# Kernel tuning notes

Measured on AMD Instinct MI355X. Metric: run time of the kernel, lower is better.

## Reference

```python
import jax, jax.numpy as jnp
import numpy as np

B, H, FEAT = 16384, 256, 256
GX, GY, SW = 70, 70, 2


def setup_inputs() -> dict:
    key = jax.random.key(0)
    ks = jax.random.split(key, 10)
    stdv = 1.0 / np.sqrt(H)
    feats = jax.random.normal(ks[0], (B, FEAT), dtype=jnp.float32)
    coords = jax.random.randint(ks[1], (B, 2), 0, 64).astype(jnp.float32)
    input_tensor = jnp.concatenate([feats, coords], axis=1)  # [B, FEAT+2]
    hidden = jax.random.normal(ks[2], (B, H), dtype=jnp.float32)
    u = lambda k, shp: jax.random.uniform(k, shp, jnp.float32, -stdv, stdv)
    return {
        "input_tensor": input_tensor,
        "hidden": hidden,
        "w_ih": u(ks[3], (4 * H, FEAT)),
        "b_ih": u(ks[4], (4 * H,)),
        "w_hh": u(ks[5], (4 * H, H)),
        "b_hh": u(ks[6], (4 * H,)),
        "w_out": u(ks[7], (H, 2 * H)),
        "b_out": u(ks[8], (H,)),
        "memory": jax.random.normal(ks[9], (GX, GY, H), dtype=jnp.float32) * 0.1,
    }


def reference(input_tensor, hidden, w_ih, b_ih, w_hh, b_hh, w_out, b_out, memory):
    feature = input_tensor[:, :-2]
    grid = input_tensor[:, -2:].astype(jnp.int32) + SW  # [B,2]

    gi = feature @ w_ih.T + b_ih  # [B,4H]
    gh = hidden @ w_hh.T + b_hh   # [B,4H]
    i_r, i_i, i_n, i_s = jnp.split(gi, 4, axis=1)
    h_r, h_i, h_n, h_s = jnp.split(gh, 4, axis=1)

    resetgate = jax.nn.sigmoid(i_r + h_r)
    updategate = jax.nn.sigmoid(i_i + h_i)
    spatialgate = jax.nn.sigmoid(i_s + h_s)
    newgate = jnp.tanh(i_n + resetgate * h_n)

    # gather (2*SW+1)^2 neighborhood per sample from spatial memory
    gx = jnp.clip(grid[:, 0], 0, GX - 1)
    gy = jnp.clip(grid[:, 1], 0, GY - 1)
    off = jnp.arange(-SW, SW + 1)  # [K]
    xi = jnp.clip(gx[:, None] + off[None, :], 0, GX - 1)  # [B,K]
    yi = jnp.clip(gy[:, None] + off[None, :], 0, GY - 1)  # [B,K]
    K = 2 * SW + 1
    x_flat = jnp.broadcast_to(xi[:, :, None], (xi.shape[0], K, K)).reshape(xi.shape[0], -1)
    y_flat = jnp.broadcast_to(yi[:, None, :], (yi.shape[0], K, K)).reshape(yi.shape[0], -1)
    context = memory[x_flat, y_flat]  # [B, K*K, H]

    # attention (query is detached in original)
    q = jax.lax.stop_gradient(newgate)  # [B,H]
    attn = jnp.einsum('bh,bkh->bk', q, context)  # [B, K*K]
    attn = jnp.where(attn == 0, -jnp.inf, attn)
    w = jax.nn.softmax(attn, axis=1)
    w = jnp.where(jnp.isnan(w), 0.0, w)
    mix = jnp.einsum('bk,bkh->bh', w, context)  # [B,H]
    combined = jnp.concatenate([mix, q], axis=1)  # [B,2H]
    atten_cs = jnp.tanh(combined @ w_out.T + b_out)  # [B,H]

    curr_state = newgate + spatialgate * atten_cs
    output = curr_state + updategate * (hidden - curr_state)
    return output
```

## Files before the change

kernel.cpp:

```cpp
#include <hip/hip_runtime.h>
#include <stdint.h>

#define B_N 16384
#define H_N 256
#define IN_W 258
#define GX_N 70
#define GY_N 70
#define SW_N 2
#define KK_N 25

typedef __bf16 bf16x8 __attribute__((ext_vector_type(8)));
typedef __bf16 bf16x4 __attribute__((ext_vector_type(4)));
typedef __bf16 bf16x2 __attribute__((ext_vector_type(2)));
typedef float f32x4 __attribute__((ext_vector_type(4)));

#define AS1 __attribute__((address_space(1)))
#define AS3 __attribute__((address_space(3)))

static __device__ __forceinline__ void gload16(const void* g, void* l) {
    __builtin_amdgcn_global_load_lds((const AS1 uint32_t*)g, (AS3 uint32_t*)l, 16, 0, 0);
}

#define E_AB   8388608ULL
#define E_WIH  8650752ULL
#define E_WHH  8912896ULL
#define E_WOUT 9043968ULL
#define E_COMB 9043968ULL
#define E_UGSG 17432576ULL

__global__ __launch_bounds__(256) void cast_kernel(
    const float* __restrict__ in_t, const float* __restrict__ hid,
    const float* __restrict__ wih, const float* __restrict__ whh,
    const float* __restrict__ wout, __bf16* __restrict__ dst)
{
    size_t g = (size_t)blockIdx.x * blockDim.x + threadIdx.x;
    size_t stride = (size_t)gridDim.x * blockDim.x;
    for (size_t e = g * 4; e < E_WOUT; e += stride * 4) {
        const float* src;
        if (e < E_AB) {
            size_t row = e >> 9;
            size_t c = e & 511;
            src = (c < 256) ? (in_t + row * IN_W + c) : (hid + row * 256 + (c - 256));
        } else if (e < E_WIH) {
            src = wih + (e - E_AB);
        } else if (e < E_WHH) {
            src = whh + (e - E_WIH);
        } else {
            src = wout + (e - E_WHH);
        }
        bf16x4 o;
        o.x = (__bf16)src[0];
        o.y = (__bf16)src[1];
        o.z = (__bf16)src[2];
        o.w = (__bf16)src[3];
        *reinterpret_cast<bf16x4*>(dst + e) = o;
    }
}

__global__ __launch_bounds__(256, 2) void gates_gemm(
    const __bf16* __restrict__ AB, const __bf16* __restrict__ wihB,
    const __bf16* __restrict__ whhB, const float* __restrict__ b_ih,
    const float* __restrict__ b_hh, __bf16* __restrict__ comb,
    __bf16* __restrict__ ugsg)
{
    __shared__ __bf16 ldsAf[4096], ldsAh[4096], ldsBi[4096], ldsBh[4096];
    const int t = threadIdx.x;
    const int lane = t & 63, w = t >> 6;
    const int lr = lane & 15, seg = lane >> 4;
    const int h0 = blockIdx.x * 32;
    const int rb = blockIdx.y * 128;

    const int r_s = t & 127;
    const int s_lo = t >> 7;
    const __bf16* gAf = AB + (size_t)(rb + r_s) * 512 + s_lo * 8;
    const __bf16* gAh = gAf + 256;
    const int wr = ((r_s >> 5) << 8) + h0 + (r_s & 31);
    const __bf16* gBi = wihB + (size_t)wr * 256 + s_lo * 8;
    const __bf16* gBh = whhB + (size_t)wr * 256 + s_lo * 8;
    __bf16* lAf = ldsAf + t * 8;
    __bf16* lAh = ldsAh + t * 8;
    __bf16* lBi = ldsBi + t * 8;
    __bf16* lBh = ldsBh + t * 8;

    f32x4 acc_i[2][4][2], acc_h[2][4][2];
#pragma unroll
    for (int rh = 0; rh < 2; rh++)
#pragma unroll
        for (int c = 0; c < 4; c++)
#pragma unroll
            for (int hh = 0; hh < 2; hh++) {
                acc_i[rh][c][hh] = (f32x4){0.f, 0.f, 0.f, 0.f};
                acc_h[rh][c][hh] = (f32x4){0.f, 0.f, 0.f, 0.f};
            }

    for (int kt = 0; kt < 256; kt += 32) {
        gload16(gAf + kt, lAf);       gload16(gAf + kt + 16, lAf + 2048);
        gload16(gAh + kt, lAh);       gload16(gAh + kt + 16, lAh + 2048);
        gload16(gBi + kt, lBi);       gload16(gBi + kt + 16, lBi + 2048);
        gload16(gBh + kt, lBh);       gload16(gBh + kt + 16, lBh + 2048);
        __syncthreads();

        bf16x8 af[2], ah[2];
#pragma unroll
        for (int rh = 0; rh < 2; rh++) {
            int tr = w * 32 + rh * 16 + lr;
            af[rh] = *reinterpret_cast<const bf16x8*>(ldsAf + seg * 1024 + tr * 8);
            ah[rh] = *reinterpret_cast<const bf16x8*>(ldsAh + seg * 1024 + tr * 8);
        }
#pragma unroll
        for (int c = 0; c < 4; c++)
#pragma unroll
            for (int hh = 0; hh < 2; hh++) {
                int br = c * 32 + hh * 16 + lr;
                bf16x8 bi = *reinterpret_cast<const bf16x8*>(ldsBi + seg * 1024 + br * 8);
                bf16x8 bh = *reinterpret_cast<const bf16x8*>(ldsBh + seg * 1024 + br * 8);
#pragma unroll
                for (int rh = 0; rh < 2; rh++) {
                    acc_i[rh][c][hh] = __builtin_amdgcn_mfma_f32_16x16x32_bf16(af[rh], bi, acc_i[rh][c][hh], 0, 0, 0);
                    acc_h[rh][c][hh] = __builtin_amdgcn_mfma_f32_16x16x32_bf16(ah[rh], bh, acc_h[rh][c][hh], 0, 0, 0);
                }
            }
        __syncthreads();
    }

#pragma unroll
    for (int hh = 0; hh < 2; hh++) {
        int col = h0 + hh * 16 + lr;
        float b0i = b_ih[col],       b0h = b_hh[col];
        float b1i = b_ih[col + 256], b1h = b_hh[col + 256];
        float b2i = b_ih[col + 512], b2h = b_hh[col + 512];
        float b3i = b_ih[col + 768], b3h = b_hh[col + 768];
#pragma unroll
        for (int rh = 0; rh < 2; rh++) {
#pragma unroll
            for (int r = 0; r < 4; r++) {
                int row = rb + w * 32 + rh * 16 + seg * 4 + r;
                float gir = acc_i[rh][0][hh][r] + b0i, ghr = acc_h[rh][0][hh][r] + b0h;
                float gii = acc_i[rh][1][hh][r] + b1i, ghi = acc_h[rh][1][hh][r] + b1h;
                float gin = acc_i[rh][2][hh][r] + b2i, ghn = acc_h[rh][2][hh][r] + b2h;
                float gis = acc_i[rh][3][hh][r] + b3i, ghs = acc_h[rh][3][hh][r] + b3h;
                float rg = 1.f / (1.f + __expf(-(gir + ghr)));
                float ug = 1.f / (1.f + __expf(-(gii + ghi)));
                float sg = 1.f / (1.f + __expf(-(gis + ghs)));
                float ng = tanhf(gin + rg * ghn);
                size_t idx = (size_t)row * 256 + col;
                comb[(size_t)row * 512 + 256 + col] = (__bf16)ng;
                bf16x2 us;
                us.x = (__bf16)ug;
                us.y = (__bf16)sg;
                *reinterpret_cast<bf16x2*>(ugsg + idx * 2) = us;
            }
        }
    }
}

__global__ __launch_bounds__(256) void attn_kernel(
    const float* __restrict__ in_t, const float* __restrict__ memory,
    __bf16* __restrict__ comb)
{
    const int w = threadIdx.x >> 6;
    const int lane = threadIdx.x & 63;
    const int b = blockIdx.x * 4 + w;
    const float* row_in = in_t + (size_t)b * IN_W;
    int gx = (int)row_in[256] + SW_N;
    int gy = (int)row_in[257] + SW_N;
    gx = min(max(gx, 0), GX_N - 1);
    gy = min(max(gy, 0), GY_N - 1);

    float q[4];
#pragma unroll
    for (int t4 = 0; t4 < 4; t4++)
        q[t4] = (float)comb[(size_t)b * 512 + 256 + t4 * 64 + lane];

    float ctx[KK_N][4];
    float attn[KK_N];
#pragma unroll
    for (int k = 0; k < KK_N; k++) {
        int i = k / 5, j = k % 5;
        int xi = min(max(gx + i - SW_N, 0), GX_N - 1);
        int yj = min(max(gy + j - SW_N, 0), GY_N - 1);
        const float* cp = memory + ((size_t)xi * GY_N + yj) * H_N;
        float p = 0.f;
#pragma unroll
        for (int t4 = 0; t4 < 4; t4++) {
            float v = cp[t4 * 64 + lane];
            ctx[k][t4] = v;
            p += q[t4] * v;
        }
        for (int off = 32; off; off >>= 1) p += __shfl_xor(p, off, 64);
        attn[k] = p;
    }

    float mval = -INFINITY;
#pragma unroll
    for (int k = 0; k < KK_N; k++) {
        float a = (attn[k] == 0.f) ? -INFINITY : attn[k];
        attn[k] = a;
        mval = fmaxf(mval, a);
    }
    float mix[4] = {0.f, 0.f, 0.f, 0.f};
    if (mval != -INFINITY) {
        float den = 0.f;
#pragma unroll
        for (int k = 0; k < KK_N; k++) {
            float e = __expf(attn[k] - mval);
            attn[k] = e;
            den += e;
        }
        float inv = 1.f / den;
#pragma unroll
        for (int k = 0; k < KK_N; k++) {
            float wk = attn[k] * inv;
#pragma unroll
            for (int t4 = 0; t4 < 4; t4++) mix[t4] += wk * ctx[k][t4];
        }
    }
    __bf16* outrow = comb + (size_t)b * 512;
#pragma unroll
    for (int t4 = 0; t4 < 4; t4++)
        outrow[t4 * 64 + lane] = (__bf16)mix[t4];
}

__global__ __launch_bounds__(256, 4) void out_gemm(
    const __bf16* __restrict__ comb, const __bf16* __restrict__ woB,
    const float* __restrict__ b_out, const __bf16* __restrict__ ugsg,
    const float* __restrict__ hidden, float* __restrict__ out)
{
    __shared__ __bf16 ldsA[4096], ldsB[2048];
    const int t = threadIdx.x;
    const int lane = t & 63, w = t >> 6;
    const int lr = lane & 15, seg = lane >> 4;
    const int n0 = blockIdx.x * 64;
    const int rb = blockIdx.y * 128;

    const int rA = t & 127;
    const int sA = t >> 7;
    const __bf16* gA = comb + (size_t)(rb + rA) * 512 + sA * 8;
    __bf16* lA = ldsA + t * 8;
    const __bf16* gB = woB + (size_t)(n0 + (t & 63)) * 512 + (t >> 6) * 8;
    __bf16* lB = ldsB + t * 8;

    f32x4 acc[2][4];
#pragma unroll
    for (int rh = 0; rh < 2; rh++)
#pragma unroll
        for (int ct = 0; ct < 4; ct++) acc[rh][ct] = (f32x4){0.f, 0.f, 0.f, 0.f};

    for (int kt = 0; kt < 512; kt += 32) {
        gload16(gA + kt, lA);
        gload16(gA + kt + 16, lA + 2048);
        gload16(gB + kt, lB);
        __syncthreads();

        bf16x8 af[2];
#pragma unroll
        for (int rh = 0; rh < 2; rh++) {
            int tr = w * 32 + rh * 16 + lr;
            af[rh] = *reinterpret_cast<const bf16x8*>(ldsA + seg * 1024 + tr * 8);
        }
#pragma unroll
        for (int ct = 0; ct < 4; ct++) {
            bf16x8 bb = *reinterpret_cast<const bf16x8*>(ldsB + seg * 512 + (ct * 16 + lr) * 8);
#pragma unroll
            for (int rh = 0; rh < 2; rh++)
                acc[rh][ct] = __builtin_amdgcn_mfma_f32_16x16x32_bf16(af[rh], bb, acc[rh][ct], 0, 0, 0);
        }
        __syncthreads();
    }

#pragma unroll
    for (int ct = 0; ct < 4; ct++) {
        int col = n0 + ct * 16 + lr;
        float bo = b_out[col];
#pragma unroll
        for (int rh = 0; rh < 2; rh++) {
#pragma unroll
            for (int r = 0; r < 4; r++) {
                int row = rb + w * 32 + rh * 16 + seg * 4 + r;
                size_t idx = (size_t)row * 256 + col;
                float acs = tanhf(acc[rh][ct][r] + bo);
                float ng = (float)comb[(size_t)row * 512 + 256 + col];
                bf16x2 us = *reinterpret_cast<const bf16x2*>(ugsg + idx * 2);
                float ug = (float)us.x, sg = (float)us.y;
                float curr = ng + sg * acs;
                out[idx] = curr + ug * (hidden[idx] - curr);
            }
        }
    }
}

extern "C" void kernel_launch(void* const* d_in, const int* in_sizes, int n_in,
                              void* d_out, int out_size, void* d_ws, size_t ws_size,
                              hipStream_t stream) {
    const float* input_t = (const float*)d_in[0];
    const float* hidden  = (const float*)d_in[1];
    const float* w_ih    = (const float*)d_in[2];
    const float* b_ih    = (const float*)d_in[3];
    const float* w_hh    = (const float*)d_in[4];
    const float* b_hh    = (const float*)d_in[5];
    const float* w_out   = (const float*)d_in[6];
    const float* b_out   = (const float*)d_in[7];
    const float* memory  = (const float*)d_in[8];
    float* out = (float*)d_out;

    __bf16* base  = (__bf16*)d_ws;
    __bf16* AB    = base;
    __bf16* wihB  = base + E_AB;
    __bf16* whhB  = base + E_WIH;
    __bf16* woutB = base + E_WHH;
    __bf16* comb  = base + E_COMB;
    __bf16* ugsg  = base + E_UGSG;

    cast_kernel<<<4096, 256, 0, stream>>>(input_t, hidden, w_ih, w_hh, w_out, base);
    gates_gemm<<<dim3(8, 128), 256, 0, stream>>>(AB, wihB, whhB, b_ih, b_hh, comb, ugsg);
    attn_kernel<<<4096, 256, 0, stream>>>(input_t, memory, comb);
    out_gemm<<<dim3(4, 128), 256, 0, stream>>>(comb, woutB, b_out, ugsg, hidden, out);
}
```

Baseline: 217.1 us.

## Fuse ih/hh gate GEMMs into one K=512 GEMM and stream attention softmax

New measurement: 209.5 us. 1.04x faster.

```diff
diff --git a/kernel.cpp b/kernel.cpp
--- a/kernel.cpp
+++ b/kernel.cpp
@@ -22,8 +22,7 @@
 }
 
 #define E_AB   8388608ULL
-#define E_WIH  8650752ULL
-#define E_WHH  8912896ULL
+#define E_WF   8912896ULL
 #define E_WOUT 9043968ULL
 #define E_COMB 9043968ULL
 #define E_UGSG 17432576ULL
@@ -41,12 +40,17 @@
             size_t row = e >> 9;
             size_t c = e & 511;
             src = (c < 256) ? (in_t + row * IN_W + c) : (hid + row * 256 + (c - 256));
-        } else if (e < E_WIH) {
-            src = wih + (e - E_AB);
-        } else if (e < E_WHH) {
-            src = whh + (e - E_WIH);
+        } else if (e < E_WF) {
+            size_t off = e - E_AB;
+            size_t j = off >> 9;
+            size_t k = off & 511;
+            size_t c = j >> 8;
+            size_t col = j & 255;
+            size_t base = (c == 0) ? 0 : (c == 1) ? 256 : (c == 2) ? 768 : 512;
+            const float* srcm = (k < 256) ? wih : whh;
+            src = srcm + (base + col) * 256 + (k & 255);
         } else {
-            src = wout + (e - E_WHH);
+            src = wout + (e - E_WF);
         }
         bf16x4 o;
         o.x = (__bf16)src[0];
@@ -57,98 +61,99 @@
     }
 }
 
-__global__ __launch_bounds__(256, 2) void gates_gemm(
-    const __bf16* __restrict__ AB, const __bf16* __restrict__ wihB,
-    const __bf16* __restrict__ whhB, const float* __restrict__ b_ih,
-    const float* __restrict__ b_hh, __bf16* __restrict__ comb,
-    __bf16* __restrict__ ugsg)
+__global__ __launch_bounds__(256, 3) void gates_gemm(
+    const __bf16* __restrict__ AB, const __bf16* __restrict__ wfull,
+    const float* __restrict__ b_ih, const float* __restrict__ b_hh,
+    __bf16* __restrict__ comb, __bf16* __restrict__ ugsg)
 {
-    __shared__ __bf16 ldsAf[4096], ldsAh[4096], ldsBi[4096], ldsBh[4096];
+    __shared__ __bf16 ldsA[4096], ldsB[4096];
     const int t = threadIdx.x;
     const int lane = t & 63, w = t >> 6;
     const int lr = lane & 15, seg = lane >> 4;
-    const int h0 = blockIdx.x * 32;
-    const int rb = blockIdx.y * 128;
+    const int rb = blockIdx.x * 128;
+    const int h0 = blockIdx.y * 32;
 
     const int r_s = t & 127;
     const int s_lo = t >> 7;
-    const __bf16* gAf = AB + (size_t)(rb + r_s) * 512 + s_lo * 8;
-    const __bf16* gAh = gAf + 256;
+    const __bf16* gA = AB + (size_t)(rb + r_s) * 512 + s_lo * 8;
     const int wr = ((r_s >> 5) << 8) + h0 + (r_s & 31);
-    const __bf16* gBi = wihB + (size_t)wr * 256 + s_lo * 8;
-    const __bf16* gBh = whhB + (size_t)wr * 256 + s_lo * 8;
-    __bf16* lAf = ldsAf + t * 8;
-    __bf16* lAh = ldsAh + t * 8;
-    __bf16* lBi = ldsBi + t * 8;
-    __bf16* lBh = ldsBh + t * 8;
-
-    f32x4 acc_i[2][4][2], acc_h[2][4][2];
-#pragma unroll
-    for (int rh = 0; rh < 2; rh++)
-#pragma unroll
-        for (int c = 0; c < 4; c++)
-#pragma unroll
-            for (int hh = 0; hh < 2; hh++) {
-                acc_i[rh][c][hh] = (f32x4){0.f, 0.f, 0.f, 0.f};
-                acc_h[rh][c][hh] = (f32x4){0.f, 0.f, 0.f, 0.f};
+    const __bf16* gB = wfull + (size_t)wr * 512 + s_lo * 8;
+    __bf16* lA = ldsA + t * 8;
+    __bf16* lB = ldsB + t * 8;
+
+    f32x4 acc_s[3][2][2], acc_ni[2][2], acc_nh[2][2];
+#pragma unroll
+    for (int hh = 0; hh < 2; hh++)
+#pragma unroll
+        for (int rh = 0; rh < 2; rh++) {
+#pragma unroll
+            for (int c = 0; c < 3; c++) acc_s[c][hh][rh] = (f32x4){0.f, 0.f, 0.f, 0.f};
+            acc_ni[hh][rh] = (f32x4){0.f, 0.f, 0.f, 0.f};
+            acc_nh[hh][rh] = (f32x4){0.f, 0.f, 0.f, 0.f};
+        }
+
+#pragma unroll 1
+    for (int half = 0; half < 2; half++) {
+        for (int kt = half * 256; kt < half * 256 + 256; kt += 32) {
+            gload16(gA + kt, lA);
+            gload16(gA + kt + 16, lA + 2048);
+            gload16(gB + kt, lB);
+            gload16(gB + kt + 16, lB + 2048);
+            __syncthreads();
+
+            bf16x8 af[2];
+#pragma unroll
+            for (int rh = 0; rh < 2; rh++) {
+                int tr = w * 32 + rh * 16 + lr;
+                af[rh] = *reinterpret_cast<const bf16x8*>(ldsA + seg * 1024 + tr * 8);
             }
-
-    for (int kt = 0; kt < 256; kt += 32) {
-        gload16(gAf + kt, lAf);       gload16(gAf + kt + 16, lAf + 2048);
-        gload16(gAh + kt, lAh);       gload16(gAh + kt + 16, lAh + 2048);
-        gload16(gBi + kt, lBi);       gload16(gBi + kt + 16, lBi + 2048);
-        gload16(gBh + kt, lBh);       gload16(gBh + kt + 16, lBh + 2048);
-        __syncthreads();
-
-        bf16x8 af[2], ah[2];
-#pragma unroll
-        for (int rh = 0; rh < 2; rh++) {
-            int tr = w * 32 + rh * 16 + lr;
-            af[rh] = *reinterpret_cast<const bf16x8*>(ldsAf + seg * 1024 + tr * 8);
-            ah[rh] = *reinterpret_cast<const bf16x8*>(ldsAh + seg * 1024 + tr * 8);
-        }
-#pragma unroll
-        for (int c = 0; c < 4; c++)
-#pragma unroll
-            for (int hh = 0; hh < 2; hh++) {
-                int br = c * 32 + hh * 16 + lr;
-                bf16x8 bi = *reinterpret_cast<const bf16x8*>(ldsBi + seg * 1024 + br * 8);
-                bf16x8 bh = *reinterpret_cast<const bf16x8*>(ldsBh + seg * 1024 + br * 8);
-#pragma unroll
-                for (int rh = 0; rh < 2; rh++) {
-                    acc_i[rh][c][hh] = __builtin_amdgcn_mfma_f32_16x16x32_bf16(af[rh], bi, acc_i[rh][c][hh], 0, 0, 0);
-                    acc_h[rh][c][hh] = __builtin_amdgcn_mfma_f32_16x16x32_bf16(ah[rh], bh, acc_h[rh][c][hh], 0, 0, 0);
+#pragma unroll
+            for (int c = 0; c < 4; c++)
+#pragma unroll
+                for (int hh = 0; hh < 2; hh++) {
+                    int br = c * 32 + hh * 16 + lr;
+                    bf16x8 bb = *reinterpret_cast<const bf16x8*>(ldsB + seg * 1024 + br * 8);
+#pragma unroll
+                    for (int rh = 0; rh < 2; rh++) {
+                        if (c < 3)
+                            acc_s[c][hh][rh] = __builtin_amdgcn_mfma_f32_16x16x32_bf16(af[rh], bb, acc_s[c][hh][rh], 0, 0, 0);
+                        else if (half == 0)
+                            acc_ni[hh][rh] = __builtin_amdgcn_mfma_f32_16x16x32_bf16(af[rh], bb, acc_ni[hh][rh], 0, 0, 0);
+                        else
+                            acc_nh[hh][rh] = __builtin_amdgcn_mfma_f32_16x16x32_bf16(af[rh], bb, acc_nh[hh][rh], 0, 0, 0);
+                    }
                 }
-            }
-        __syncthreads();
+            __syncthreads();
+        }
     }
 
 #pragma unroll
     for (int hh = 0; hh < 2; hh++) {
         int col = h0 + hh * 16 + lr;
-        float b0i = b_ih[col],       b0h = b_hh[col];
-        float b1i = b_ih[col + 256], b1h = b_hh[col + 256];
-        float b2i = b_ih[col + 512], b2h = b_hh[col + 512];
-        float b3i = b_ih[col + 768], b3h = b_hh[col + 768];
+        float br_ = b_ih[col] + b_hh[col];
+        float bi_ = b_ih[col + 256] + b_hh[col + 256];
+        float bs_ = b_ih[col + 768] + b_hh[col + 768];
+        float bni = b_ih[col + 512];
+        float bnh = b_hh[col + 512];
 #pragma unroll
         for (int rh = 0; rh < 2; rh++) {
 #pragma unroll
             for (int r = 0; r < 4; r++) {
                 int row = rb + w * 32 + rh * 16 + seg * 4 + r;
-                float gir = acc_i[rh][0][hh][r] + b0i, ghr = acc_h[rh][0][hh][r] + b0h;
-                float gii = acc_i[rh][1][hh][r] + b1i, ghi = acc_h[rh][1][hh][r] + b1h;
-                float gin = acc_i[rh][2][hh][r] + b2i, ghn = acc_h[rh][2][hh][r] + b2h;
-                float gis = acc_i[rh][3][hh][r] + b3i, ghs = acc_h[rh][3][hh][r] + b3h;
-                float rg = 1.f / (1.f + __expf(-(gir + ghr)));
-                float ug = 1.f / (1.f + __expf(-(gii + ghi)));
-                float sg = 1.f / (1.f + __expf(-(gis + ghs)));
-                float ng = tanhf(gin + rg * ghn);
-                size_t idx = (size_t)row * 256 + col;
+                float sr = acc_s[0][hh][rh][r] + br_;
+                float si = acc_s[1][hh][rh][r] + bi_;
+                float ss = acc_s[2][hh][rh][r] + bs_;
+                float ni = acc_ni[hh][rh][r] + bni;
+                float nh = acc_nh[hh][rh][r] + bnh;
+                float rg = 1.f / (1.f + __expf(-sr));
+                float ug = 1.f / (1.f + __expf(-si));
+                float sg = 1.f / (1.f + __expf(-ss));
+                float ng = tanhf(ni + rg * nh);
                 comb[(size_t)row * 512 + 256 + col] = (__bf16)ng;
                 bf16x2 us;
                 us.x = (__bf16)ug;
                 us.y = (__bf16)sg;
-                *reinterpret_cast<bf16x2*>(ugsg + idx * 2) = us;
+                *reinterpret_cast<bf16x2*>(ugsg + ((size_t)row * 256 + col) * 2) = us;
             }
         }
     }
@@ -167,58 +172,40 @@
     gx = min(max(gx, 0), GX_N - 1);
     gy = min(max(gy, 0), GY_N - 1);
 
-    float q[4];
-#pragma unroll
-    for (int t4 = 0; t4 < 4; t4++)
-        q[t4] = (float)comb[(size_t)b * 512 + 256 + t4 * 64 + lane];
-
-    float ctx[KK_N][4];
-    float attn[KK_N];
+    bf16x4 qb = *reinterpret_cast<const bf16x4*>(comb + (size_t)b * 512 + 256 + lane * 4);
+    float q0 = (float)qb.x, q1 = (float)qb.y, q2 = (float)qb.z, q3 = (float)qb.w;
+
+    float m = -INFINITY, d = 0.f;
+    float o0 = 0.f, o1 = 0.f, o2 = 0.f, o3 = 0.f;
 #pragma unroll
     for (int k = 0; k < KK_N; k++) {
         int i = k / 5, j = k % 5;
         int xi = min(max(gx + i - SW_N, 0), GX_N - 1);
         int yj = min(max(gy + j - SW_N, 0), GY_N - 1);
-        const float* cp = memory + ((size_t)xi * GY_N + yj) * H_N;
-        float p = 0.f;
-#pragma unroll
-        for (int t4 = 0; t4 < 4; t4++) {
-            float v = cp[t4 * 64 + lane];
-            ctx[k][t4] = v;
-            p += q[t4] * v;
-        }
+        const f32x4* cp = reinterpret_cast<const f32x4*>(memory + ((size_t)xi * GY_N + yj) * H_N);
+        f32x4 v = cp[lane];
+        float p = q0 * v.x + q1 * v.y + q2 * v.z + q3 * v.w;
         for (int off = 32; off; off >>= 1) p += __shfl_xor(p, off, 64);
-        attn[k] = p;
-    }
-
-    float mval = -INFINITY;
-#pragma unroll
-    for (int k = 0; k < KK_N; k++) {
-        float a = (attn[k] == 0.f) ? -INFINITY : attn[k];
-        attn[k] = a;
-        mval = fmaxf(mval, a);
-    }
-    float mix[4] = {0.f, 0.f, 0.f, 0.f};
-    if (mval != -INFINITY) {
-        float den = 0.f;
-#pragma unroll
-        for (int k = 0; k < KK_N; k++) {
-            float e = __expf(attn[k] - mval);
-            attn[k] = e;
-            den += e;
-        }
-        float inv = 1.f / den;
-#pragma unroll
-        for (int k = 0; k < KK_N; k++) {
-            float wk = attn[k] * inv;
-#pragma unroll
-            for (int t4 = 0; t4 < 4; t4++) mix[t4] += wk * ctx[k][t4];
-        }
-    }
-    __bf16* outrow = comb + (size_t)b * 512;
-#pragma unroll
-    for (int t4 = 0; t4 < 4; t4++)
-        outrow[t4 * 64 + lane] = (__bf16)mix[t4];
+        float a = (p == 0.f) ? -INFINITY : p;
+        float mn = fmaxf(m, a);
+        if (mn != -INFINITY) {
+            float alpha = __expf(m - mn);
+            float e = __expf(a - mn);
+            d = d * alpha + e;
+            o0 = o0 * alpha + e * v.x;
+            o1 = o1 * alpha + e * v.y;
+            o2 = o2 * alpha + e * v.z;
+            o3 = o3 * alpha + e * v.w;
+            m = mn;
+        }
+    }
+    float inv = (d != 0.f) ? 1.f / d : 0.f;
+    bf16x4 ob;
+    ob.x = (__bf16)(o0 * inv);
+    ob.y = (__bf16)(o1 * inv);
+    ob.z = (__bf16)(o2 * inv);
+    ob.w = (__bf16)(o3 * inv);
+    *reinterpret_cast<bf16x4*>(comb + (size_t)b * 512 + lane * 4) = ob;
 }
 
 __global__ __launch_bounds__(256, 4) void out_gemm(
@@ -230,8 +217,8 @@
     const int t = threadIdx.x;
     const int lane = t & 63, w = t >> 6;
     const int lr = lane & 15, seg = lane >> 4;
-    const int n0 = blockIdx.x * 64;
-    const int rb = blockIdx.y * 128;
+    const int rb = blockIdx.x * 128;
+    const int n0 = blockIdx.y * 64;
 
     const int rA = t & 127;
     const int sA = t >> 7;
@@ -305,14 +292,13 @@
 
     __bf16* base  = (__bf16*)d_ws;
     __bf16* AB    = base;
-    __bf16* wihB  = base + E_AB;
-    __bf16* whhB  = base + E_WIH;
-    __bf16* woutB = base + E_WHH;
+    __bf16* wfull = base + E_AB;
+    __bf16* woutB = base + E_WF;
     __bf16* comb  = base + E_COMB;
     __bf16* ugsg  = base + E_UGSG;
 
     cast_kernel<<<4096, 256, 0, stream>>>(input_t, hidden, w_ih, w_hh, w_out, base);
-    gates_gemm<<<dim3(8, 128), 256, 0, stream>>>(AB, wihB, whhB, b_ih, b_hh, comb, ugsg);
+    gates_gemm<<<dim3(128, 8), 256, 0, stream>>>(AB, wfull, b_ih, b_hh, comb, ugsg);
     attn_kernel<<<4096, 256, 0, stream>>>(input_t, memory, comb);
-    out_gemm<<<dim3(4, 128), 256, 0, stream>>>(comb, woutB, b_out, ugsg, hidden, out);
-}
+    out_gemm<<<dim3(128, 4), 256, 0, stream>>>(comb, woutB, b_out, ugsg, hidden, out);
+}
```
